# Optimization experiments

Hardware: AMD Instinct MI355X
Metric: run time of the kernel (lower is better)

## Reference

```python
import jax, jax.numpy as jnp
import numpy as np

NUM_GRAPHS = 512  # number of segments (graphs) in the batch
NEG_SLOPE = 0.01  # nn.LeakyReLU default


def setup_inputs() -> dict:
    key = jax.random.key(0)
    k1, k2, k3, k4, k5 = jax.random.split(key, 5)
    N, D = 200000, 128
    h_topo = jax.random.normal(k1, (N, D), dtype=jnp.float32)
    h_geom = jax.random.normal(k2, (N, D), dtype=jnp.float32)
    batch = jnp.sort(jax.random.randint(k3, (N,), 0, NUM_GRAPHS, dtype=jnp.int64))
    concat_dim, hidden, out_dim = 6 * D, 2 * D, 128
    W1 = jax.random.normal(k4, (concat_dim, hidden), dtype=jnp.float32) * 0.02
    b1 = jnp.zeros((hidden,), dtype=jnp.float32)
    W2 = jax.random.normal(k5, (hidden, out_dim), dtype=jnp.float32) * 0.02
    b2 = jnp.zeros((out_dim,), dtype=jnp.float32)
    return {"h_topo": h_topo, "h_geom": h_geom, "batch": batch,
            "W1": W1, "b1": b1, "W2": W2, "b2": b2}


def _pool_feats(h, batch):
    # global_max_pool / global_mean_pool keyed by graph id, gathered back per node
    gmax = jax.ops.segment_max(h, batch, num_segments=NUM_GRAPHS)
    gsum = jax.ops.segment_sum(h, batch, num_segments=NUM_GRAPHS)
    cnt = jax.ops.segment_sum(jnp.ones((h.shape[0],), h.dtype), batch,
                              num_segments=NUM_GRAPHS)
    gmean = gsum / jnp.maximum(cnt, 1.0)[:, None]
    return gmax[batch], gmean[batch]  # [N, D] each


def reference(h_topo, h_geom, batch, W1, b1, W2, b2):
    t_max, t_mean = _pool_feats(h_topo, batch)
    g_max, g_mean = _pool_feats(h_geom, batch)
    # [Topo, Geom, TopoMax, TopoMean, GeomMax, GeomMean]
    combined = jnp.concatenate(
        [h_topo, t_max, t_mean, h_geom, g_max, g_mean], axis=-1)  # [N, 6D]
    h = combined @ W1 + b1
    h = jnp.where(h >= 0, h, NEG_SLOPE * h)  # LeakyReLU
    return h @ W2 + b2
```

## Files before the change

kernel.cpp:

```cpp
#include <hip/hip_runtime.h>
#include <math.h>

#define NUM_GRAPHS 512
#define D 128
#define NEG 0.01f
#define BN 128
#define NS 4

typedef __attribute__((ext_vector_type(8))) short  bf16x8;
typedef __attribute__((ext_vector_type(4))) float  f32x4;
typedef __attribute__((ext_vector_type(4))) int    i32x4;

__device__ __forceinline__ unsigned short f2bf(float f) {
    unsigned u = __float_as_uint(f);
    u += 0x7fffu + ((u >> 16) & 1u);
    return (unsigned short)(u >> 16);
}

__device__ __forceinline__ bf16x8 cvt8(float4 a, float4 b) {
    unsigned w0, w1, w2, w3;
    asm("v_cvt_pk_bf16_f32 %0, %1, %2" : "=v"(w0) : "v"(a.x), "v"(a.y));
    asm("v_cvt_pk_bf16_f32 %0, %1, %2" : "=v"(w1) : "v"(a.z), "v"(a.w));
    asm("v_cvt_pk_bf16_f32 %0, %1, %2" : "=v"(w2) : "v"(b.x), "v"(b.y));
    asm("v_cvt_pk_bf16_f32 %0, %1, %2" : "=v"(w3) : "v"(b.z), "v"(b.w));
    i32x4 v; v[0] = (int)w0; v[1] = (int)w1; v[2] = (int)w2; v[3] = (int)w3;
    return __builtin_bit_cast(bf16x8, v);
}

__device__ __forceinline__ int swz128(int row, int k) {
    return (row >> 6) * 16384 + (row & 63) * 256 + (k ^ ((row & 7) << 3));
}

#define LDS_BARRIER()                                                        \
    do {                                                                     \
        asm volatile("s_waitcnt lgkmcnt(0)" ::: "memory");                   \
        __builtin_amdgcn_s_barrier();                                        \
        asm volatile("" ::: "memory");                                       \
    } while (0)

#define FMAX4(a, b)                                                          \
    do {                                                                     \
        (a).x = fmaxf((a).x, (b).x); (a).y = fmaxf((a).y, (b).y);            \
        (a).z = fmaxf((a).z, (b).z); (a).w = fmaxf((a).w, (b).w);            \
    } while (0)
#define FADD4(a, b)                                                          \
    do {                                                                     \
        (a).x += (b).x; (a).y += (b).y; (a).z += (b).z; (a).w += (b).w;      \
    } while (0)

__global__ __launch_bounds__(256) void bounds_kernel(
    const int* __restrict__ batch, int N, int* __restrict__ seg)
{
    const int g = blockIdx.x * 256 + threadIdx.x;
    if (g <= NUM_GRAPHS) {
        int lo = 0, hi = N;
        while (lo < hi) { int m = (lo + hi) >> 1; if (batch[m] < g) lo = m + 1; else hi = m; }
        seg[g] = lo;
    }
}

__global__ __launch_bounds__(256) void pool_kernel(
    const float* __restrict__ h_topo, const float* __restrict__ h_geom,
    const int* __restrict__ seg, int N, float* __restrict__ pp)
{
    const int g = blockIdx.x, t = blockIdx.y, s = blockIdx.z;
    const float* __restrict__ h = t ? h_geom : h_topo;

    const int start = seg[g], end = seg[g + 1];
    const int len = end - start;
    const int r0  = start + (int)(((long long)len * s) / NS);
    const int r1  = start + (int)(((long long)len * (s + 1)) / NS);

    const int c = threadIdx.x & 31;
    const int r = threadIdx.x >> 5;

    float4 mxA = make_float4(-INFINITY, -INFINITY, -INFINITY, -INFINITY);
    float4 mxB = mxA, mxC = mxA, mxD = mxA;
    float4 smA = make_float4(0.f, 0.f, 0.f, 0.f);
    float4 smB = smA, smC = smA, smD = smA;

    int row = r0 + r;
    for (; row + 24 < r1; row += 32) {
        float4 v0 = *(const float4*)(h + (size_t)row * D + c * 4);
        float4 v1 = *(const float4*)(h + (size_t)(row + 8)  * D + c * 4);
        float4 v2 = *(const float4*)(h + (size_t)(row + 16) * D + c * 4);
        float4 v3 = *(const float4*)(h + (size_t)(row + 24) * D + c * 4);
        FMAX4(mxA, v0); FADD4(smA, v0);
        FMAX4(mxB, v1); FADD4(smB, v1);
        FMAX4(mxC, v2); FADD4(smC, v2);
        FMAX4(mxD, v3); FADD4(smD, v3);
    }
    for (; row < r1; row += 8) {
        float4 v = *(const float4*)(h + (size_t)row * D + c * 4);
        FMAX4(mxA, v); FADD4(smA, v);
    }
    FMAX4(mxA, mxB); FMAX4(mxC, mxD); FMAX4(mxA, mxC);
    FADD4(smA, smB); FADD4(smC, smD); FADD4(smA, smC);

    __shared__ float4 smx[256], ssm[256];
    smx[threadIdx.x] = mxA; ssm[threadIdx.x] = smA;
    __syncthreads();
    #pragma unroll
    for (int st = 4; st > 0; st >>= 1) {
        if (r < st) {
            float4 a = smx[threadIdx.x + st * 32];
            float4 b = ssm[threadIdx.x + st * 32];
            float4 m0 = smx[threadIdx.x];
            float4 s0 = ssm[threadIdx.x];
            FMAX4(m0, a); FADD4(s0, b);
            smx[threadIdx.x] = m0; ssm[threadIdx.x] = s0;
        }
        __syncthreads();
    }
    if (r == 0) {
        float* dst = pp + ((size_t)(g * 2 + t) * NS + s) * 256;
        *(float4*)(dst + c * 4)       = smx[threadIdx.x];
        *(float4*)(dst + 128 + c * 4) = ssm[threadIdx.x];
    }
}

__global__ __launch_bounds__(256) void pmat_kernel(
    const float* __restrict__ pp, const int* __restrict__ seg,
    const float* __restrict__ W1, const float* __restrict__ b1,
    float* __restrict__ P)
{
    const int g = blockIdx.x;
    const int j = threadIdx.x;

    const int start = seg[g], end = seg[g + 1];
    const float inv   = 1.0f / fmaxf((float)(end - start), 1.0f);
    const bool  empty = (end <= start);

    __shared__ float pl[512];
    #pragma unroll
    for (int e0 = 0; e0 < 2; ++e0) {
        const int e = j + e0 * 256;
        const int t = e >> 8, i = e & 255;
        const float* q = pp + (size_t)(g * 2 + t) * NS * 256 + i;
        float v;
        if (i < 128)
            v = fmaxf(fmaxf(q[0], q[256]), fmaxf(q[512], q[768]));
        else
            v = (q[0] + q[256] + q[512] + q[768]) * inv;
        pl[e] = empty ? 0.f : v;
    }
    __syncthreads();

    float acc = b1[j];
    #pragma unroll 8
    for (int k = 0; k < 256; ++k)
        acc += pl[k] * W1[(size_t)(128 + k) * 256 + j];
    #pragma unroll 8
    for (int k = 0; k < 256; ++k)
        acc += pl[256 + k] * W1[(size_t)(512 + k) * 256 + j];

    P[(size_t)g * 256 + j] = acc;
}

__global__ __launch_bounds__(256) void wconv_kernel(
    const float* __restrict__ W1, const float* __restrict__ W2,
    unsigned short* __restrict__ W1bT, unsigned short* __restrict__ W2bT)
{
    const int idx = blockIdx.x * 256 + threadIdx.x;
    if (idx < 256 * 256) {
        const int n = idx >> 8, k = idx & 255;
        const int kk = (k < 128) ? k : (k + 256);
        W1bT[idx] = f2bf(W1[(size_t)kk * 256 + n]);
    } else {
        const int j = idx - 256 * 256;
        if (j < 128 * 256) {
            const int n = j >> 8, k = j & 255;
            W2bT[j] = f2bf(W2[(size_t)k * 128 + n]);
        }
    }
}

__global__ __launch_bounds__(512, 4) void mlp_mfma(
    const float* __restrict__ h_topo, const float* __restrict__ h_geom,
    const int* __restrict__ batch, const float* __restrict__ P,
    const unsigned short* __restrict__ W1bT, const unsigned short* __restrict__ W2bT,
    const float* __restrict__ b2, float* __restrict__ out, int N)
{
    __shared__ unsigned short xs[128 * 256];
    __shared__ int gid[128];

    const int tid  = threadIdx.x;
    const int wave = tid >> 6, lane = tid & 63;
    const int base = blockIdx.x * BN;

    {
        const int row  = tid >> 2, kq = tid & 3;
        const int node = min(base + row, N - 1);
        const float* src = (kq < 2) ? h_topo + (size_t)node * D + kq * 64
                                    : h_geom + (size_t)node * D + (kq - 2) * 64;
        #pragma unroll
        for (int i = 0; i < 8; ++i) {
            float4 a = ((const float4*)src)[2 * i];
            float4 b = ((const float4*)src)[2 * i + 1];
            *(bf16x8*)&xs[swz128(row, kq * 64 + i * 8)] = cvt8(a, b);
        }
    }
    if (tid < 128) gid[tid] = batch[min(base + tid, N - 1)];

    const int g0 = batch[base];
    const int g1 = batch[min(base + 127, N - 1)];
    const bool uni = (g0 == g1);

    const int lhi = lane >> 4;
    const int llo = lane & 15;

    const unsigned short* w1p = W1bT + (size_t)(wave * 32 + llo) * 256 + lhi * 8;
    const unsigned short* w2p = W2bT + (size_t)(wave * 16 + llo) * 256 + lhi * 8;

    float pf[2];
    if (uni) {
        #pragma unroll
        for (int ct = 0; ct < 2; ++ct)
            pf[ct] = P[(size_t)g0 * 256 + wave * 32 + ct * 16 + llo];
    }

    bf16x8 bfr[2][2];
    #pragma unroll
    for (int ct = 0; ct < 2; ++ct) {
        bfr[0][ct] = *(const bf16x8*)(w1p + (size_t)ct * 16 * 256);
        bfr[1][ct] = *(const bf16x8*)(w1p + (size_t)ct * 16 * 256 + 32);
    }

    LDS_BARRIER();

    f32x4 acc[8][2];
    #pragma unroll
    for (int rt = 0; rt < 8; ++rt)
        #pragma unroll
        for (int ct = 0; ct < 2; ++ct) {
            const float p = uni ? pf[ct] : 0.f;
            acc[rt][ct] = (f32x4){p, p, p, p};
        }

    #pragma unroll
    for (int ks = 0; ks < 8; ++ks) {
        const int kb = ks * 32 + lhi * 8;
        bf16x8 afr[8];
        #pragma unroll
        for (int rt = 0; rt < 8; ++rt)
            afr[rt] = *(const bf16x8*)&xs[swz128(rt * 16 + llo, kb)];
        __builtin_amdgcn_s_setprio(1);
        #pragma unroll
        for (int rt = 0; rt < 8; ++rt)
            #pragma unroll
            for (int ct = 0; ct < 2; ++ct)
                acc[rt][ct] = __builtin_amdgcn_mfma_f32_16x16x32_bf16(
                    afr[rt], bfr[ks & 1][ct], acc[rt][ct], 0, 0, 0);
        __builtin_amdgcn_s_setprio(0);
        if (ks < 6) {
            const int kbn = (ks + 2) * 32;
            #pragma unroll
            for (int ct = 0; ct < 2; ++ct)
                bfr[ks & 1][ct] = *(const bf16x8*)(w1p + (size_t)ct * 16 * 256 + kbn);
        }
    }

    bf16x8 bfr2[2];
    bfr2[0] = *(const bf16x8*)(w2p);
    bfr2[1] = *(const bf16x8*)(w2p + 32);

    LDS_BARRIER();

    #pragma unroll
    for (int rt = 0; rt < 8; ++rt) {
        #pragma unroll
        for (int ct = 0; ct < 2; ++ct) {
            const int col = wave * 32 + ct * 16 + llo;
            #pragma unroll
            for (int q = 0; q < 4; ++q) {
                const int row = rt * 16 + lhi * 4 + q;
                float v = acc[rt][ct][q];
                if (!uni) v += P[(size_t)gid[row] * 256 + col];
                v = fmaxf(v, NEG * v);
                xs[swz128(row, col)] = f2bf(v);
            }
        }
    }

    LDS_BARRIER();

    f32x4 acc2[8];
    {
        const float4 bb = *(const float4*)(b2 + wave * 16 + lhi * 4);
        #pragma unroll
        for (int rt = 0; rt < 8; ++rt)
            acc2[rt] = (f32x4){bb.x, bb.y, bb.z, bb.w};
    }
    #pragma unroll
    for (int ks = 0; ks < 8; ++ks) {
        const int kb = ks * 32 + lhi * 8;
        bf16x8 hfr[8];
        #pragma unroll
        for (int rt = 0; rt < 8; ++rt)
            hfr[rt] = *(const bf16x8*)&xs[swz128(rt * 16 + llo, kb)];
        __builtin_amdgcn_s_setprio(1);
        #pragma unroll
        for (int rt = 0; rt < 8; ++rt)
            acc2[rt] = __builtin_amdgcn_mfma_f32_16x16x32_bf16(
                bfr2[ks & 1], hfr[rt], acc2[rt], 0, 0, 0);
        __builtin_amdgcn_s_setprio(0);
        if (ks < 6)
            bfr2[ks & 1] = *(const bf16x8*)(w2p + (ks + 2) * 32);
    }

    #pragma unroll
    for (int rt = 0; rt < 8; ++rt) {
        const int node = base + rt * 16 + llo;
        if (node < N)
            __builtin_nontemporal_store(
                acc2[rt],
                (f32x4*)(out + (size_t)node * 128 + wave * 16 + lhi * 4));
    }
}

extern "C" void kernel_launch(void* const* d_in, const int* in_sizes, int n_in,
                              void* d_out, int out_size, void* d_ws, size_t ws_size,
                              hipStream_t stream)
{
    const float* h_topo = (const float*)d_in[0];
    const float* h_geom = (const float*)d_in[1];
    const int*   batch  = (const int*)  d_in[2];
    const float* W1     = (const float*)d_in[3];
    const float* b1     = (const float*)d_in[4];
    const float* W2     = (const float*)d_in[5];
    const float* b2     = (const float*)d_in[6];
    float* out = (float*)d_out;

    const int N = in_sizes[0] / D;

    float*          pp   = (float*)d_ws;
    float*          P    = pp + (size_t)NUM_GRAPHS * 2 * NS * 256;
    unsigned short* W1bT = (unsigned short*)(P + (size_t)NUM_GRAPHS * 256);
    unsigned short* W2bT = W1bT + 256 * 256;
    int*            seg  = (int*)(W2bT + 128 * 256);

    bounds_kernel<<<3, 256, 0, stream>>>(batch, N, seg);
    wconv_kernel<<<(256 * 256 + 128 * 256) / 256, 256, 0, stream>>>(W1, W2, W1bT, W2bT);
    pool_kernel<<<dim3(NUM_GRAPHS, 2, NS), 256, 0, stream>>>(h_topo, h_geom, seg, N, pp);
    pmat_kernel<<<NUM_GRAPHS, 256, 0, stream>>>(pp, seg, W1, b1, P);

    const int nblocks = (N + BN - 1) / BN;
    mlp_mfma<<<nblocks, 512, 0, stream>>>(h_topo, h_geom, batch, P,
                                          W1bT, W2bT, b2, out, N);
}
```

Before: 169.4 us.

## Retile second GEMM per wave to 4 row tiles by 2 column tiles, reverse block order

```diff
diff --git a/kernel.cpp b/kernel.cpp
--- a/kernel.cpp
+++ b/kernel.cpp
@@ -186,7 +186,7 @@
 
     const int tid  = threadIdx.x;
     const int wave = tid >> 6, lane = tid & 63;
-    const int base = blockIdx.x * BN;
+    const int base = (gridDim.x - 1 - blockIdx.x) * BN;
 
     {
         const int row  = tid >> 2, kq = tid & 3;
@@ -210,7 +210,6 @@
     const int llo = lane & 15;
 
     const unsigned short* w1p = W1bT + (size_t)(wave * 32 + llo) * 256 + lhi * 8;
-    const unsigned short* w2p = W2bT + (size_t)(wave * 16 + llo) * 256 + lhi * 8;
 
     float pf[2];
     if (uni) {
@@ -260,9 +259,15 @@
         }
     }
 
-    bf16x8 bfr2[2];
-    bfr2[0] = *(const bf16x8*)(w2p);
-    bfr2[1] = *(const bf16x8*)(w2p + 32);
+    const int jp = wave & 3, ng = wave >> 2;
+    const unsigned short* w2pA = W2bT + (size_t)((2 * jp)     * 16 + llo) * 256 + lhi * 8;
+    const unsigned short* w2pB = W2bT + (size_t)((2 * jp + 1) * 16 + llo) * 256 + lhi * 8;
+
+    bf16x8 bfr2[2][2];
+    bfr2[0][0] = *(const bf16x8*)(w2pA);
+    bfr2[0][1] = *(const bf16x8*)(w2pB);
+    bfr2[1][0] = *(const bf16x8*)(w2pA + 32);
+    bfr2[1][1] = *(const bf16x8*)(w2pB + 32);
 
     LDS_BARRIER();
 
@@ -284,37 +289,46 @@
 
     LDS_BARRIER();
 
-    f32x4 acc2[8];
+    f32x4 acc2[4][2];
     {
-        const float4 bb = *(const float4*)(b2 + wave * 16 + lhi * 4);
-        #pragma unroll
-        for (int rt = 0; rt < 8; ++rt)
-            acc2[rt] = (f32x4){bb.x, bb.y, bb.z, bb.w};
+        const float4 bbA = *(const float4*)(b2 + (2 * jp)     * 16 + lhi * 4);
+        const float4 bbB = *(const float4*)(b2 + (2 * jp + 1) * 16 + lhi * 4);
+        #pragma unroll
+        for (int nt = 0; nt < 4; ++nt) {
+            acc2[nt][0] = (f32x4){bbA.x, bbA.y, bbA.z, bbA.w};
+            acc2[nt][1] = (f32x4){bbB.x, bbB.y, bbB.z, bbB.w};
+        }
     }
     #pragma unroll
     for (int ks = 0; ks < 8; ++ks) {
         const int kb = ks * 32 + lhi * 8;
-        bf16x8 hfr[8];
-        #pragma unroll
-        for (int rt = 0; rt < 8; ++rt)
-            hfr[rt] = *(const bf16x8*)&xs[swz128(rt * 16 + llo, kb)];
+        bf16x8 hfr[4];
+        #pragma unroll
+        for (int nt = 0; nt < 4; ++nt)
+            hfr[nt] = *(const bf16x8*)&xs[swz128((ng * 4 + nt) * 16 + llo, kb)];
         __builtin_amdgcn_s_setprio(1);
         #pragma unroll
-        for (int rt = 0; rt < 8; ++rt)
-            acc2[rt] = __builtin_amdgcn_mfma_f32_16x16x32_bf16(
-                bfr2[ks & 1], hfr[rt], acc2[rt], 0, 0, 0);
+        for (int nt = 0; nt < 4; ++nt) {
+            acc2[nt][0] = __builtin_amdgcn_mfma_f32_16x16x32_bf16(
+                bfr2[ks & 1][0], hfr[nt], acc2[nt][0], 0, 0, 0);
+            acc2[nt][1] = __builtin_amdgcn_mfma_f32_16x16x32_bf16(
+                bfr2[ks & 1][1], hfr[nt], acc2[nt][1], 0, 0, 0);
+        }
         __builtin_amdgcn_s_setprio(0);
-        if (ks < 6)
-            bfr2[ks & 1] = *(const bf16x8*)(w2p + (ks + 2) * 32);
-    }
-
-    #pragma unroll
-    for (int rt = 0; rt < 8; ++rt) {
-        const int node = base + rt * 16 + llo;
-        if (node < N)
-            __builtin_nontemporal_store(
-                acc2[rt],
-                (f32x4*)(out + (size_t)node * 128 + wave * 16 + lhi * 4));
+        if (ks < 6) {
+            bfr2[ks & 1][0] = *(const bf16x8*)(w2pA + (ks + 2) * 32);
+            bfr2[ks & 1][1] = *(const bf16x8*)(w2pB + (ks + 2) * 32);
+        }
+    }
+
+    #pragma unroll
+    for (int nt = 0; nt < 4; ++nt) {
+        const int node = base + (ng * 4 + nt) * 16 + llo;
+        if (node < N) {
+            float* op = out + (size_t)node * 128 + jp * 32 + lhi * 4;
+            __builtin_nontemporal_store(acc2[nt][0], (f32x4*)op);
+            __builtin_nontemporal_store(acc2[nt][1], (f32x4*)(op + 16));
+        }
     }
 }
 
```

Result: slower. 175.2 us (+3.4%).
